# Kernel optimization log

Hardware: AMD Instinct MI355X
Metric: run time of the kernel (lower is better)

Reference implementation:

```python
import jax, jax.numpy as jnp
import numpy as np

COMMITMENT = 0.25
THRESHOLD = 0.6
SNR_DB = 30.0  # eval_snr_db default-ish channel condition (fixed for determinism)
LN_EPS = 1e-5


def _layernorm(x, g, b):
    m = jnp.mean(x, axis=-1, keepdims=True)
    v = jnp.var(x, axis=-1, keepdims=True)
    return (x - m) * jax.lax.rsqrt(v + LN_EPS) * g + b


def _vq(x, codebook):
    # x: [T, D], codebook: [K, D]. Nearest-neighbor quantize + per-token VQ loss + STE.
    d = (x * x).sum(-1, keepdims=True) - 2.0 * (x @ codebook.T) + (codebook * codebook).sum(-1)  # [T, K]
    idx = jnp.argmin(d, axis=-1)
    q = codebook[idx]  # [T, D]
    loss = (COMMITMENT * jnp.mean((x - jax.lax.stop_gradient(q)) ** 2, axis=-1)
            + jnp.mean((jax.lax.stop_gradient(x) - q) ** 2, axis=-1))  # [T]
    q_ste = x + jax.lax.stop_gradient(q - x)
    return q_ste, loss


def setup_inputs() -> dict:
    key = jax.random.key(0)
    ks = jax.random.split(key, 8)
    B, N, De, Dq, Dd = 64, 196, 768, 512, 256
    return {
        'x_tokens': jax.random.normal(ks[0], (B, N, De), jnp.float32),
        'fim_logits': jax.random.normal(ks[1], (B, N, 1), jnp.float32),
        'W_proj': jax.random.normal(ks[2], (De, Dq), jnp.float32) * (1.0 / np.sqrt(De)),
        'b_proj': jnp.zeros((Dq,), jnp.float32),
        'ln_g': jnp.ones((Dq,), jnp.float32),
        'ln_b': jnp.zeros((Dq,), jnp.float32),
        'cb_high': jax.random.normal(ks[3], (4096, Dq), jnp.float32),
        'cb_low': jax.random.normal(ks[4], (256, Dq), jnp.float32),
        'W_dec': jax.random.normal(ks[5], (Dq, Dd), jnp.float32) * (1.0 / np.sqrt(Dq)),
        'b_dec': jnp.zeros((Dd,), jnp.float32),
        'h_ri': jax.random.normal(ks[6], (B, 2), jnp.float32),
        'noise': jax.random.normal(ks[7], (B, N, Dq), jnp.float32),
    }


def reference(x_tokens, fim_logits, W_proj, b_proj, ln_g, ln_b, cb_high, cb_low, W_dec, b_dec, h_ri, noise):
    B, N, _ = x_tokens.shape
    score = jax.nn.sigmoid(fim_logits[..., 0])          # [B, N]
    route_high = score > THRESHOLD                       # [B, N] bool

    x_proj = _layernorm(x_tokens @ W_proj + b_proj, ln_g, ln_b)  # [B, N, Dq]
    D = x_proj.shape[-1]
    xf = x_proj.reshape(-1, D)
    mf = route_high.reshape(-1)
    sf = score.reshape(-1)

    # Compute both experts densely, select with mask (same math as the masked
    # gather/scatter dispatch in the torch code, jit-friendly static shapes).
    q_high, loss_high = _vq(xf, cb_high)
    q_low, loss_low = _vq(xf, cb_low)
    final = jnp.where(mf[:, None], q_high, q_low).reshape(B, N, D)

    n_high = jnp.maximum(mf.sum(), 1)
    n_low = jnp.maximum((~mf).sum(), 1)
    vq_loss = (jnp.sum(jnp.where(mf, loss_high * sf, 0.0)) / n_high
               + jnp.sum(jnp.where(mf, 0.0, loss_low * (1.0 - sf))) / n_low) / 2.0

    # Rayleigh channel: per-sample fading magnitude h = |CN(0,1)|/sqrt(2), AWGN, equalize.
    n_var = 10.0 ** (-SNR_DB / 10.0)
    h = jnp.sqrt((h_ri ** 2).sum(-1)) / jnp.sqrt(2.0)    # [B]
    h = h[:, None, None]
    y = (h * final + jnp.sqrt(n_var) * noise) / h

    x_dec = y @ W_dec + b_dec                            # [B, N, 256]
    return x_dec, vq_loss
```

## Files before the change

### kernel.cpp

```cpp
#include <hip/hip_runtime.h>
#include <math.h>

#define T_TOK 12544
#define DE 768
#define DQ 512
#define DD 256
#define SEQ 196
#define NCH 4096
#define NCL 256
#define SPL_H 16
#define CODES_PER_BLK 256
#define MARGIN 2.0f
#define CAND_CAP 16

typedef __attribute__((ext_vector_type(8))) short s16x8;
typedef __attribute__((ext_vector_type(4))) float f32x4;

__device__ __forceinline__ float wave_reduce_sum(float v) {
    #pragma unroll
    for (int off = 32; off > 0; off >>= 1) v += __shfl_xor(v, off);
    return v;
}

__device__ __forceinline__ unsigned short f2bf(float f) {
    unsigned int u = __float_as_uint(f);
    u = (u + 0x7fffu + ((u >> 16) & 1u)) >> 16;
    return (unsigned short)u;
}
__device__ __forceinline__ float bf2f(unsigned short h) {
    return __uint_as_float(((unsigned int)h) << 16);
}

__device__ __forceinline__ void sumsq_body(const float* __restrict__ cb,
                                           float* __restrict__ cs2,
                                           unsigned short* __restrict__ cbB,
                                           int blk, int NC) {
    int row = blk * 4 + (threadIdx.x >> 6);
    int lane = threadIdx.x & 63;
    if (row >= NC) return;
    const float4* p = (const float4*)(cb + (size_t)row * DQ);
    float4 a = p[lane];
    float4 b = p[lane + 64];
    if (cbB) {
        unsigned short* dst = cbB + (size_t)row * DQ;
        ushort4 ha, hb;
        ha.x = f2bf(a.x); ha.y = f2bf(a.y); ha.z = f2bf(a.z); ha.w = f2bf(a.w);
        hb.x = f2bf(b.x); hb.y = f2bf(b.y); hb.z = f2bf(b.z); hb.w = f2bf(b.w);
        *(ushort4*)(dst + lane * 4) = ha;
        *(ushort4*)(dst + 256 + lane * 4) = hb;
    }
    float s = a.x*a.x + a.y*a.y + a.z*a.z + a.w*a.w
            + b.x*b.x + b.y*b.y + b.z*b.z + b.w*b.w;
    s = wave_reduce_sum(s);
    if (lane == 0) cs2[row] = s;
}

__device__ __forceinline__ void split_body(const float* __restrict__ W, int K, int N,
                                           unsigned short* __restrict__ Thi,
                                           unsigned short* __restrict__ Tlo,
                                           int blk, int nb) {
    int total = K * N;
    for (int idx = blk * 256 + threadIdx.x; idx < total; idx += nb * 256) {
        int n = idx / K, k = idx - n * K;
        float v = W[(size_t)k * N + n];
        unsigned short h = f2bf(v);
        Thi[idx] = h;
        Tlo[idx] = f2bf(v - bf2f(h));
    }
}

__global__ __launch_bounds__(256) void prep_all(const float* __restrict__ cb_h,
                                                float* __restrict__ cs2h,
                                                unsigned short* __restrict__ cbhB,
                                                const float* __restrict__ cb_l,
                                                float* __restrict__ cs2l,
                                                unsigned short* __restrict__ cblB,
                                                const float* __restrict__ Wp,
                                                unsigned short* __restrict__ WThi,
                                                unsigned short* __restrict__ WTlo,
                                                const float* __restrict__ Wd,
                                                unsigned short* __restrict__ WdThi,
                                                unsigned short* __restrict__ WdTlo) {
    int blk = blockIdx.x;
    if (blk < 1024)       sumsq_body(cb_h, cs2h, cbhB, blk, NCH);
    else if (blk < 1088)  sumsq_body(cb_l, cs2l, cblB, blk - 1024, NCL);
    else if (blk < 1600)  split_body(Wp, DE, DQ, WThi, WTlo, blk - 1088, 512);
    else                  split_body(Wd, DQ, DD, WdThi, WdTlo, blk - 1600, 256);
}

template<int NC>
__global__ __launch_bounds__(256) void code_sumsq(const float* __restrict__ cb,
                                                  float* __restrict__ cs2) {
    sumsq_body(cb, cs2, nullptr, blockIdx.x, NC);
}

template<int KDIM, int NSTRIDE, int BN>
__global__ __launch_bounds__(256) void gemm_mfma3(const float* __restrict__ A,
                                                  const unsigned short* __restrict__ BThi,
                                                  const unsigned short* __restrict__ BTlo,
                                                  const float* __restrict__ bias,
                                                  float* __restrict__ out) {
    constexpr int CPW = BN / 64;
    __shared__ __align__(16) unsigned short Ahi[2][64 * 32];
    __shared__ __align__(16) unsigned short Alo[2][64 * 32];
    __shared__ __align__(16) unsigned short Bhi[2][BN * 32];
    __shared__ __align__(16) unsigned short Blo[2][BN * 32];
    const int m0 = blockIdx.x * 64, n0 = blockIdx.y * BN;
    const int tid = threadIdx.x, lane = tid & 63, w = tid >> 6;
    const int stok = tid >> 2, sslot = tid & 3;

    f32x4 acc[4][CPW] = {};
    float4 av0, av1;
    uint4 bh4[CPW], bl4[CPW];

    auto loadStep = [&](int k0) {
        const float* src = A + (size_t)(m0 + stok) * KDIM + k0 + sslot * 8;
        av0 = *(const float4*)src;
        av1 = *(const float4*)(src + 4);
        #pragma unroll
        for (int c = 0; c < CPW; c++) {
            size_t soff = (size_t)(n0 + c * 64 + stok) * KDIM + k0 + sslot * 8;
            bh4[c] = *(const uint4*)(BThi + soff);
            bl4[c] = *(const uint4*)(BTlo + soff);
        }
    };
    auto writeStep = [&](int buf) {
        float xv[8] = {av0.x, av0.y, av0.z, av0.w, av1.x, av1.y, av1.z, av1.w};
        unsigned int hw[4], lw[4];
        #pragma unroll
        for (int j = 0; j < 4; j++) {
            unsigned short h0 = f2bf(xv[2*j]),   h1 = f2bf(xv[2*j+1]);
            unsigned short l0 = f2bf(xv[2*j] - bf2f(h0));
            unsigned short l1 = f2bf(xv[2*j+1] - bf2f(h1));
            hw[j] = (unsigned)h0 | ((unsigned)h1 << 16);
            lw[j] = (unsigned)l0 | ((unsigned)l1 << 16);
        }
        int doffA = stok * 32 + (sslot ^ ((stok >> 1) & 3)) * 8;
        *(uint4*)&Ahi[buf][doffA] = make_uint4(hw[0], hw[1], hw[2], hw[3]);
        *(uint4*)&Alo[buf][doffA] = make_uint4(lw[0], lw[1], lw[2], lw[3]);
        #pragma unroll
        for (int c = 0; c < CPW; c++) {
            int col = c * 64 + stok;
            int doffB = col * 32 + (sslot ^ ((col >> 1) & 3)) * 8;
            *(uint4*)&Bhi[buf][doffB] = bh4[c];
            *(uint4*)&Blo[buf][doffB] = bl4[c];
        }
    };

    loadStep(0); writeStep(0); __syncthreads();
    const int NT = KDIM / 32;
    for (int t = 0; t < NT; t++) {
        const int cur = t & 1;
        if (t + 1 < NT) loadStep((t + 1) * 32);
        const int fr = lane & 15, fs = lane >> 4;
        s16x8 ah[4], al[4];
        #pragma unroll
        for (int tm = 0; tm < 4; tm++) {
            int tok = tm * 16 + fr;
            int off = tok * 32 + (fs ^ ((tok >> 1) & 3)) * 8;
            ah[tm] = *(const s16x8*)&Ahi[cur][off];
            al[tm] = *(const s16x8*)&Alo[cur][off];
        }
        #pragma unroll
        for (int n = 0; n < CPW; n++) {
            int col = w * (16 * CPW) + n * 16 + fr;
            int boff = col * 32 + (fs ^ ((col >> 1) & 3)) * 8;
            s16x8 bh = *(const s16x8*)&Bhi[cur][boff];
            s16x8 bl = *(const s16x8*)&Blo[cur][boff];
            #pragma unroll
            for (int tm = 0; tm < 4; tm++) {
                acc[tm][n] = __builtin_amdgcn_mfma_f32_16x16x32_bf16(ah[tm], bh, acc[tm][n], 0, 0, 0);
                acc[tm][n] = __builtin_amdgcn_mfma_f32_16x16x32_bf16(ah[tm], bl, acc[tm][n], 0, 0, 0);
                acc[tm][n] = __builtin_amdgcn_mfma_f32_16x16x32_bf16(al[tm], bh, acc[tm][n], 0, 0, 0);
            }
        }
        if (t + 1 < NT) writeStep(cur ^ 1);
        __syncthreads();
    }
    const int fr = lane & 15, fg = lane >> 4;
    #pragma unroll
    for (int n = 0; n < CPW; n++) {
        const int col = n0 + w * (16 * CPW) + n * 16 + fr;
        const float bb = bias[col];
        #pragma unroll
        for (int tm = 0; tm < 4; tm++) {
            #pragma unroll
            for (int r = 0; r < 4; r++) {
                int row = m0 + tm * 16 + fg * 4 + r;
                out[(size_t)row * NSTRIDE + col] = acc[tm][n][r] + bb;
            }
        }
    }
}

__global__ __launch_bounds__(256) void proj_gemm(const float* __restrict__ X,
                                                 const float* __restrict__ W,
                                                 const float* __restrict__ bias,
                                                 float* __restrict__ out) {
    __shared__ float As[32][66];
    __shared__ float Bs[32][64];
    const int m0 = blockIdx.x * 64, n0 = blockIdx.y * 64;
    const int tid = threadIdx.x;
    const int tx = tid & 15, ty = tid >> 4;
    float acc[4][4] = {};
    for (int k0 = 0; k0 < DE; k0 += 32) {
        {
            int e = tid;
            int r = e >> 3, c4 = e & 7;
            float4 v = *(const float4*)(X + (size_t)(m0 + r) * DE + k0 + c4 * 4);
            As[c4*4+0][r] = v.x; As[c4*4+1][r] = v.y; As[c4*4+2][r] = v.z; As[c4*4+3][r] = v.w;
            e = tid + 256;
            r = e >> 3; c4 = e & 7;
            v = *(const float4*)(X + (size_t)(m0 + r) * DE + k0 + c4 * 4);
            As[c4*4+0][r] = v.x; As[c4*4+1][r] = v.y; As[c4*4+2][r] = v.z; As[c4*4+3][r] = v.w;
        }
        {
            int e = tid;
            int kk = e >> 4, c4 = e & 15;
            *(float4*)&Bs[kk][c4*4] = *(const float4*)(W + (size_t)(k0 + kk) * DQ + n0 + c4 * 4);
            e = tid + 256;
            kk = e >> 4; c4 = e & 15;
            *(float4*)&Bs[kk][c4*4] = *(const float4*)(W + (size_t)(k0 + kk) * DQ + n0 + c4 * 4);
        }
        __syncthreads();
        #pragma unroll
        for (int k = 0; k < 32; k++) {
            float2 a01 = *(const float2*)&As[k][ty * 4];
            float2 a23 = *(const float2*)&As[k][ty * 4 + 2];
            float4 b = *(const float4*)&Bs[k][tx * 4];
            float av[4] = {a01.x, a01.y, a23.x, a23.y};
            float bv[4] = {b.x, b.y, b.z, b.w};
            #pragma unroll
            for (int i = 0; i < 4; i++)
                #pragma unroll
                for (int j = 0; j < 4; j++)
                    acc[i][j] += av[i] * bv[j];
        }
        __syncthreads();
    }
    float4 bv4 = *(const float4*)(bias + n0 + tx * 4);
    float bb[4] = {bv4.x, bv4.y, bv4.z, bv4.w};
    #pragma unroll
    for (int i = 0; i < 4; i++) {
        int row = m0 + ty * 4 + i;
        float4 o;
        o.x = acc[i][0] + bb[0];
        o.y = acc[i][1] + bb[1];
        o.z = acc[i][2] + bb[2];
        o.w = acc[i][3] + bb[3];
        *(float4*)(out + (size_t)row * DQ + n0 + tx * 4) = o;
    }
}

__global__ __launch_bounds__(256) void ln_route(float* __restrict__ xp,
                                                const float* __restrict__ g,
                                                const float* __restrict__ b,
                                                const float* __restrict__ logits,
                                                float* __restrict__ score,
                                                int* __restrict__ mask,
                                                unsigned short* __restrict__ xpB) {
    int row = blockIdx.x * 4 + (threadIdx.x >> 6);
    int lane = threadIdx.x & 63;
    float* p = xp + (size_t)row * DQ;
    float4 v0 = *(float4*)(p + lane * 4);
    float4 v1 = *(float4*)(p + 256 + lane * 4);
    float s  = v0.x + v0.y + v0.z + v0.w + v1.x + v1.y + v1.z + v1.w;
    float ss = v0.x*v0.x + v0.y*v0.y + v0.z*v0.z + v0.w*v0.w
             + v1.x*v1.x + v1.y*v1.y + v1.z*v1.z + v1.w*v1.w;
    s = wave_reduce_sum(s);
    ss = wave_reduce_sum(ss);
    float m = s * (1.f / DQ);
    float var = ss * (1.f / DQ) - m * m;
    float scale = rsqrtf(var + 1e-5f);
    float4 g0 = *(const float4*)(g + lane * 4);
    float4 g1 = *(const float4*)(g + 256 + lane * 4);
    float4 b0 = *(const float4*)(b + lane * 4);
    float4 b1 = *(const float4*)(b + 256 + lane * 4);
    float4 o0, o1;
    o0.x = (v0.x - m) * scale * g0.x + b0.x;
    o0.y = (v0.y - m) * scale * g0.y + b0.y;
    o0.z = (v0.z - m) * scale * g0.z + b0.z;
    o0.w = (v0.w - m) * scale * g0.w + b0.w;
    o1.x = (v1.x - m) * scale * g1.x + b1.x;
    o1.y = (v1.y - m) * scale * g1.y + b1.y;
    o1.z = (v1.z - m) * scale * g1.z + b1.z;
    o1.w = (v1.w - m) * scale * g1.w + b1.w;
    *(float4*)(p + lane * 4) = o0;
    *(float4*)(p + 256 + lane * 4) = o1;
    if (xpB) {
        unsigned short* dst = xpB + (size_t)row * DQ;
        ushort4 h0, h1;
        h0.x = f2bf(o0.x); h0.y = f2bf(o0.y); h0.z = f2bf(o0.z); h0.w = f2bf(o0.w);
        h1.x = f2bf(o1.x); h1.y = f2bf(o1.y); h1.z = f2bf(o1.z); h1.w = f2bf(o1.w);
        *(ushort4*)(dst + lane * 4) = h0;
        *(ushort4*)(dst + 256 + lane * 4) = h1;
    }
    if (lane == 0) {
        float lg = logits[row];
        float sc = 1.f / (1.f + expf(-lg));
        score[row] = sc;
        mask[row] = sc > 0.6f ? 1 : 0;
    }
}

__global__ __launch_bounds__(1024) void scan_compact(const int* __restrict__ mask,
                                                     int* __restrict__ hlist,
                                                     int* __restrict__ llist,
                                                     int* __restrict__ counts) {
    __shared__ int wsum[16];
    __shared__ int base_h, base_l;
    int tid = threadIdx.x, lane = tid & 63, wid = tid >> 6;
    if (tid == 0) { base_h = 0; base_l = 0; }
    __syncthreads();
    for (int t0 = 0; t0 < T_TOK; t0 += 1024) {
        int t = t0 + tid;
        int valid = t < T_TOK;
        int m = valid ? mask[t] : 0;
        unsigned long long bal = __ballot(m);
        int pre = __popcll(bal & ((1ull << lane) - 1ull));
        if (lane == 0) wsum[wid] = __popcll(bal);
        __syncthreads();
        int woff = 0;
        for (int w = 0; w < wid; w++) woff += wsum[w];
        int btot = 0;
        for (int w = 0; w < 16; w++) btot += wsum[w];
        int vcnt = T_TOK - t0; if (vcnt > 1024) vcnt = 1024;
        int bh = base_h, bl = base_l;
        if (valid) {
            if (m) hlist[bh + woff + pre] = t;
            else   llist[bl + (tid - (woff + pre))] = t;
        }
        __syncthreads();
        if (tid == 0) { base_h = bh + btot; base_l = bl + (vcnt - btot); }
        __syncthreads();
    }
    if (tid == 0) { counts[0] = base_h; counts[1] = base_l; }
}

__global__ __launch_bounds__(256) void vq_mfma_all(const unsigned short* __restrict__ xpB,
                                                   const unsigned short* __restrict__ cbhB,
                                                   const float* __restrict__ cs2h,
                                                   const int* __restrict__ hlist,
                                                   const unsigned short* __restrict__ cblB,
                                                   const float* __restrict__ cs2l,
                                                   const int* __restrict__ llist,
                                                   const int* __restrict__ counts,
                                                   float* __restrict__ smaxH,
                                                   int* __restrict__ scntH,
                                                   uint2* __restrict__ candH,
                                                   float* __restrict__ smaxL,
                                                   int* __restrict__ scntL,
                                                   uint2* __restrict__ candL) {
    const int by = blockIdx.y;
    const unsigned short* cbB; const float* cs2; const int* list;
    float* smax; int* scnt; uint2* cand;
    int count, slice, SPLIT;
    if (by < SPL_H) {
        cbB = cbhB; cs2 = cs2h; list = hlist; count = counts[0];
        slice = by; SPLIT = SPL_H; smax = smaxH; scnt = scntH; cand = candH;
    } else {
        cbB = cblB; cs2 = cs2l; list = llist; count = counts[1];
        slice = 0; SPLIT = 1; smax = smaxL; scnt = scntL; cand = candL;
    }
    const int base = blockIdx.x * 64;
    if (base >= count) return;
    const int cbase = slice * CODES_PER_BLK;

    __shared__ __align__(16) unsigned short Abuf[2][64 * 32];
    __shared__ __align__(16) unsigned short Bbuf[2][256 * 32];
    __shared__ float wmaxs[4][64];
    __shared__ float tokmax[64];
    __shared__ int ccnt[64];
    __shared__ uint2 cland[64][CAND_CAP];
    __shared__ int rows_s[64];

    const int tid = threadIdx.x;
    const int lane = tid & 63;
    const int w = tid >> 6;

    if (tid < 64) {
        int tl = base + tid;
        rows_s[tid] = list[tl < count ? tl : (count - 1)];
        ccnt[tid] = 0;
    }
    __syncthreads();

    f32x4 acc[4][4] = {};

    const int stok = tid >> 2, sslot = tid & 3;
    for (int k0 = 0; k0 < DQ; k0 += 64) {
        if (k0) __syncthreads();
        #pragma unroll
        for (int h = 0; h < 2; h++) {
            uint4 v = *(const uint4*)(xpB + (size_t)rows_s[stok] * DQ + k0 + h * 32 + sslot * 8);
            *(uint4*)&Abuf[h][stok * 32 + (sslot ^ ((stok >> 1) & 3)) * 8] = v;
            #pragma unroll
            for (int cc = 0; cc < 4; cc++) {
                int code = cc * 64 + stok;
                uint4 bv = *(const uint4*)(cbB + (size_t)(cbase + code) * DQ + k0 + h * 32 + sslot * 8);
                *(uint4*)&Bbuf[h][code * 32 + (sslot ^ ((code >> 1) & 3)) * 8] = bv;
            }
        }
        __syncthreads();
        const int fr = lane & 15, fs = lane >> 4;
        #pragma unroll
        for (int h = 0; h < 2; h++) {
            s16x8 af[4], bf[4];
            #pragma unroll
            for (int tm = 0; tm < 4; tm++) {
                int tok = tm * 16 + fr;
                af[tm] = *(const s16x8*)&Abuf[h][tok * 32 + (fs ^ ((tok >> 1) & 3)) * 8];
            }
            #pragma unroll
            for (int tn = 0; tn < 4; tn++) {
                int cl = w * 64 + tn * 16 + fr;
                bf[tn] = *(const s16x8*)&Bbuf[h][cl * 32 + (fs ^ ((cl >> 1) & 3)) * 8];
            }
            #pragma unroll
            for (int tm = 0; tm < 4; tm++)
                #pragma unroll
                for (int tn = 0; tn < 4; tn++)
                    acc[tm][tn] = __builtin_amdgcn_mfma_f32_16x16x32_bf16(af[tm], bf[tn], acc[tm][tn], 0, 0, 0);
        }
    }
    __syncthreads();

    const int fr = lane & 15, fg = lane >> 4;
    float c2[4];
    #pragma unroll
    for (int tn = 0; tn < 4; tn++) c2[tn] = 0.5f * cs2[cbase + w * 64 + tn * 16 + fr];

    #pragma unroll
    for (int tm = 0; tm < 4; tm++) {
        #pragma unroll
        for (int r = 0; r < 4; r++) {
            float m4 = -3.0e38f;
            #pragma unroll
            for (int tn = 0; tn < 4; tn++) {
                float s = acc[tm][tn][r] - c2[tn];
                m4 = fmaxf(m4, s);
            }
            #pragma unroll
            for (int off = 1; off < 16; off <<= 1)
                m4 = fmaxf(m4, __shfl_xor(m4, off));
            if (fr == 0) wmaxs[w][tm * 16 + fg * 4 + r] = m4;
        }
    }
    __syncthreads();
    if (tid < 64)
        tokmax[tid] = fmaxf(fmaxf(wmaxs[0][tid], wmaxs[1][tid]),
                            fmaxf(wmaxs[2][tid], wmaxs[3][tid]));
    __syncthreads();

    #pragma unroll
    for (int tm = 0; tm < 4; tm++) {
        #pragma unroll
        for (int r = 0; r < 4; r++) {
            int token = tm * 16 + fg * 4 + r;
            float thr = tokmax[token] - MARGIN;
            #pragma unroll
            for (int tn = 0; tn < 4; tn++) {
                float s = acc[tm][tn][r] - c2[tn];
                if (s > thr) {
                    int pos = atomicAdd(&ccnt[token], 1);
                    if (pos < CAND_CAP) {
                        uint2 cd;
                        cd.x = __float_as_uint(s);
                        cd.y = (unsigned)(cbase + w * 64 + tn * 16 + fr);
                        cland[token][pos] = cd;
                    }
                }
            }
        }
    }
    __syncthreads();

    if (tid < 64) {
        int tl = base + tid;
        if (tl < count) {
            smax[(size_t)tl * SPLIT + slice] = tokmax[tid];
            scnt[(size_t)tl * SPLIT + slice] = min(ccnt[tid], CAND_CAP);
        }
    }
    for (int i = tid; i < 64 * CAND_CAP; i += 256) {
        int token = i >> 4, j = i & (CAND_CAP - 1);
        int tl = base + token;
        if (tl < count && j < min(ccnt[token], CAND_CAP))
            cand[((size_t)tl * SPLIT + slice) * CAND_CAP + j] = cland[token][j];
    }
}

__global__ __launch_bounds__(256) void vq_rescore_all(float* __restrict__ xp,
                                                      const float* __restrict__ cb_h,
                                                      const float* __restrict__ smaxH,
                                                      const int* __restrict__ scntH,
                                                      const uint2* __restrict__ candH,
                                                      const int* __restrict__ hlist,
                                                      const float* __restrict__ cb_l,
                                                      const float* __restrict__ smaxL,
                                                      const int* __restrict__ scntL,
                                                      const uint2* __restrict__ candL,
                                                      const int* __restrict__ llist,
                                                      const int* __restrict__ counts,
                                                      int* __restrict__ out_idx,
                                                      const float* __restrict__ noise,
                                                      const float* __restrict__ h_ri,
                                                      const float* __restrict__ score,
                                                      float* __restrict__ lh,
                                                      float* __restrict__ ll) {
    const int HB = T_TOK / 4;
    int bx = blockIdx.x;
    const float* cb; const float* smax; const int* scnt; const uint2* cand; const int* list;
    int count, SPLIT, cidx;
    if (bx < HB) {
        cb = cb_h; smax = smaxH; scnt = scntH; cand = candH; list = hlist;
        count = counts[0]; SPLIT = SPL_H; cidx = 0;
    } else {
        bx -= HB;
        cb = cb_l; smax = smaxL; scnt = scntL; cand = candL; list = llist;
        count = counts[1]; SPLIT = 1; cidx = 1;
    }
    const int wid = threadIdx.x >> 6;
    const int lane = threadIdx.x & 63;
    const int tl = bx * 4 + wid;
    if (tl >= count) return;

    float gm = -3.0e38f;
    if (lane < SPLIT) gm = smax[(size_t)tl * SPLIT + lane];
    #pragma unroll
    for (int off = 1; off < 64; off <<= 1)
        gm = fmaxf(gm, __shfl_xor(gm, off));
    const float thr = gm - MARGIN;

    const int t = list[tl];
    float xv[8];
    #pragma unroll
    for (int kk = 0; kk < 8; kk++) xv[kk] = xp[(size_t)t * DQ + lane * 8 + kk];

    double bs = -1.0e300;
    int bi = 0x7fffffff;
    for (int s = 0; s < SPLIT; s++) {
        int cn = scnt[(size_t)tl * SPLIT + s];
        for (int j = 0; j < cn; j++) {
            uint2 cd = cand[((size_t)tl * SPLIT + s) * CAND_CAP + j];
            float av = __uint_as_float(cd.x);
            if (av >= thr) {
                int code = (int)cd.y;
                const float* crow = cb + (size_t)code * DQ;
                double dot = 0.0, nrm = 0.0;
                #pragma unroll
                for (int kk = 0; kk < 8; kk++) {
                    double cv = (double)crow[lane * 8 + kk];
                    dot += (double)xv[kk] * cv;
                    nrm += cv * cv;
                }
                #pragma unroll
                for (int off = 1; off < 64; off <<= 1) {
                    dot += __shfl_xor(dot, off);
                    nrm += __shfl_xor(nrm, off);
                }
                double sc = dot - 0.5 * nrm;
                if (sc > bs || (sc == bs && code < bi)) { bs = sc; bi = code; }
            }
        }
    }
    const float* qrow = cb + (size_t)bi * DQ;
    float4 q0 = *(const float4*)(qrow + lane * 8);
    float4 q1 = *(const float4*)(qrow + lane * 8 + 4);
    const float* nz = noise + (size_t)t * DQ;
    float4 n0 = *(const float4*)(nz + lane * 8);
    float4 n1 = *(const float4*)(nz + lane * 8 + 4);
    float ds = 0.f, dx;
    dx = xv[0] - q0.x; ds += dx * dx;
    dx = xv[1] - q0.y; ds += dx * dx;
    dx = xv[2] - q0.z; ds += dx * dx;
    dx = xv[3] - q0.w; ds += dx * dx;
    dx = xv[4] - q1.x; ds += dx * dx;
    dx = xv[5] - q1.y; ds += dx * dx;
    dx = xv[6] - q1.z; ds += dx * dx;
    dx = xv[7] - q1.w; ds += dx * dx;
    ds = wave_reduce_sum(ds);
    int bbt = t / SEQ;
    float hh0 = h_ri[bbt * 2], hh1 = h_ri[bbt * 2 + 1];
    float hh = sqrtf((hh0 * hh0 + hh1 * hh1) * 0.5f);
    float cc = sqrtf(1e-3f) / hh;
    float4 y0, y1;
    y0.x = q0.x + cc * n0.x; y0.y = q0.y + cc * n0.y;
    y0.z = q0.z + cc * n0.z; y0.w = q0.w + cc * n0.w;
    y1.x = q1.x + cc * n1.x; y1.y = q1.y + cc * n1.y;
    y1.z = q1.z + cc * n1.z; y1.w = q1.w + cc * n1.w;
    *(float4*)(xp + (size_t)t * DQ + lane * 8) = y0;
    *(float4*)(xp + (size_t)t * DQ + lane * 8 + 4) = y1;
    if (lane == 0) {
        out_idx[t] = bi;
        float loss = 1.25f * ds * (1.f / DQ);
        float sc = score[t];
        if (cidx == 0) { lh[t] = loss * sc;  ll[t] = 0.f; }
        else           { lh[t] = 0.f;        ll[t] = loss * (1.f - sc); }
    }
}

template<int NC, int SPLIT>
__global__ __launch_bounds__(256) void vq_partial(const float* __restrict__ xp,
                                                  const float* __restrict__ cb,
                                                  const float* __restrict__ cs2,
                                                  const int* __restrict__ list,
                                                  const int* __restrict__ counts,
                                                  int cidx,
                                                  float* __restrict__ part_s,
                                                  int* __restrict__ part_i) {
    const int count = counts[cidx];
    const int base = blockIdx.x * 64;
    if (base >= count) return;
    const int CODES = NC / SPLIT;
    const int cbase = blockIdx.y * CODES;
    __shared__ float As[32][68];
    __shared__ float Cs[32][68];
    __shared__ int rows_s[64];
    const int tid = threadIdx.x;
    if (tid < 64) {
        int tl = base + tid;
        rows_s[tid] = list[tl < count ? tl : (count - 1)];
    }
    __syncthreads();
    const int tx = tid & 15, ty = tid >> 4;
    float best_s[4];
    int best_i[4];
    #pragma unroll
    for (int i = 0; i < 4; i++) { best_s[i] = -3.0e38f; best_i[i] = 0; }
    for (int c0 = cbase; c0 < cbase + CODES; c0 += 64) {
        float acc[4][4] = {};
        for (int k0 = 0; k0 < DQ; k0 += 32) {
            {
                int e = tid;
                int r = e >> 3, c4 = e & 7;
                float4 v = *(const float4*)(xp + (size_t)rows_s[r] * DQ + k0 + c4 * 4);
                As[c4*4+0][r] = v.x; As[c4*4+1][r] = v.y; As[c4*4+2][r] = v.z; As[c4*4+3][r] = v.w;
                e = tid + 256; r = e >> 3; c4 = e & 7;
                v = *(const float4*)(xp + (size_t)rows_s[r] * DQ + k0 + c4 * 4);
                As[c4*4+0][r] = v.x; As[c4*4+1][r] = v.y; As[c4*4+2][r] = v.z; As[c4*4+3][r] = v.w;
            }
            {
                int e = tid;
                int r = e >> 3, c4 = e & 7;
                float4 v = *(const float4*)(cb + (size_t)(c0 + r) * DQ + k0 + c4 * 4);
                Cs[c4*4+0][r] = v.x; Cs[c4*4+1][r] = v.y; Cs[c4*4+2][r] = v.z; Cs[c4*4+3][r] = v.w;
                e = tid + 256; r = e >> 3; c4 = e & 7;
                v = *(const float4*)(cb + (size_t)(c0 + r) * DQ + k0 + c4 * 4);
                Cs[c4*4+0][r] = v.x; Cs[c4*4+1][r] = v.y; Cs[c4*4+2][r] = v.z; Cs[c4*4+3][r] = v.w;
            }
            __syncthreads();
            #pragma unroll
            for (int k = 0; k < 32; k++) {
                float4 a = *(const float4*)&As[k][ty * 4];
                float4 b = *(const float4*)&Cs[k][tx * 4];
                float av[4] = {a.x, a.y, a.z, a.w};
                float bv[4] = {b.x, b.y, b.z, b.w};
                #pragma unroll
                for (int i = 0; i < 4; i++)
                    #pragma unroll
                    for (int j = 0; j < 4; j++)
                        acc[i][j] += av[i] * bv[j];
            }
            __syncthreads();
        }
        float4 c2v = *(const float4*)(cs2 + c0 + tx * 4);
        float c2[4] = {c2v.x, c2v.y, c2v.z, c2v.w};
        #pragma unroll
        for (int i = 0; i < 4; i++) {
            float s = acc[i][0] - 0.5f * c2[0];
            int bi = c0 + tx * 4;
            #pragma unroll
            for (int j = 1; j < 4; j++) {
                float sj = acc[i][j] - 0.5f * c2[j];
                if (sj > s) { s = sj; bi = c0 + tx * 4 + j; }
            }
            #pragma unroll
            for (int off = 1; off < 16; off <<= 1) {
                float os = __shfl_xor(s, off);
                int oi = __shfl_xor(bi, off);
                if (os > s || (os == s && oi < bi)) { s = os; bi = oi; }
            }
            if (s > best_s[i] || (s == best_s[i] && bi < best_i[i])) {
                best_s[i] = s; best_i[i] = bi;
            }
        }
    }
    if (tx == 0) {
        #pragma unroll
        for (int i = 0; i < 4; i++) {
            int tl = base + ty * 4 + i;
            if (tl < count) {
                part_s[(size_t)tl * SPLIT + blockIdx.y] = best_s[i];
                part_i[(size_t)tl * SPLIT + blockIdx.y] = best_i[i];
            }
        }
    }
}

template<int SPLIT>
__global__ __launch_bounds__(256) void vq_reduce(const float* __restrict__ part_s,
                                                 const int* __restrict__ part_i,
                                                 const int* __restrict__ list,
                                                 const int* __restrict__ counts,
                                                 int cidx,
                                                 int* __restrict__ out_idx) {
    int tl = blockIdx.x * 256 + threadIdx.x;
    if (tl >= counts[cidx]) return;
    float bs = part_s[(size_t)tl * SPLIT];
    int bi = part_i[(size_t)tl * SPLIT];
    #pragma unroll
    for (int s = 1; s < SPLIT; s++) {
        float v = part_s[(size_t)tl * SPLIT + s];
        int vi = part_i[(size_t)tl * SPLIT + s];
        if (v > bs || (v == bs && vi < bi)) { bs = v; bi = vi; }
    }
    out_idx[list[tl]] = bi;
}

__global__ __launch_bounds__(256) void gather_loss_y(float* __restrict__ xp,
                                                     const float* __restrict__ cb_h,
                                                     const float* __restrict__ cb_l,
                                                     const int* __restrict__ idx,
                                                     const float* __restrict__ score,
                                                     const int* __restrict__ mask,
                                                     const float* __restrict__ noise,
                                                     const float* __restrict__ h_ri,
                                                     float* __restrict__ lh,
                                                     float* __restrict__ ll) {
    int t = blockIdx.x * 4 + (threadIdx.x >> 6);
    int lane = threadIdx.x & 63;
    int m = mask[t];
    float sc = score[t];
    const float* q = (m ? cb_h : cb_l) + (size_t)idx[t] * DQ;
    float* x = xp + (size_t)t * DQ;
    const float* nz = noise + (size_t)t * DQ;
    int bb = t / SEQ;
    float h0 = h_ri[bb * 2], h1 = h_ri[bb * 2 + 1];
    float h = sqrtf((h0 * h0 + h1 * h1) * 0.5f);
    float c = sqrtf(1e-3f) / h;
    float4 xv0 = *(float4*)(x + lane * 4);
    float4 xv1 = *(float4*)(x + 256 + lane * 4);
    float4 qv0 = *(const float4*)(q + lane * 4);
    float4 qv1 = *(const float4*)(q + 256 + lane * 4);
    float4 nv0 = *(const float4*)(nz + lane * 4);
    float4 nv1 = *(const float4*)(nz + 256 + lane * 4);
    float dx, ds = 0.f;
    dx = xv0.x - qv0.x; ds += dx * dx;
    dx = xv0.y - qv0.y; ds += dx * dx;
    dx = xv0.z - qv0.z; ds += dx * dx;
    dx = xv0.w - qv0.w; ds += dx * dx;
    dx = xv1.x - qv1.x; ds += dx * dx;
    dx = xv1.y - qv1.y; ds += dx * dx;
    dx = xv1.z - qv1.z; ds += dx * dx;
    dx = xv1.w - qv1.w; ds += dx * dx;
    ds = wave_reduce_sum(ds);
    float4 y0, y1;
    y0.x = qv0.x + c * nv0.x; y0.y = qv0.y + c * nv0.y;
    y0.z = qv0.z + c * nv0.z; y0.w = qv0.w + c * nv0.w;
    y1.x = qv1.x + c * nv1.x; y1.y = qv1.y + c * nv1.y;
    y1.z = qv1.z + c * nv1.z; y1.w = qv1.w + c * nv1.w;
    *(float4*)(x + lane * 4) = y0;
    *(float4*)(x + 256 + lane * 4) = y1;
    if (lane == 0) {
        float loss = 1.25f * ds * (1.f / DQ);
        lh[t] = m ? loss * sc : 0.f;
        ll[t] = m ? 0.f : loss * (1.f - sc);
    }
}

__global__ __launch_bounds__(256) void loss_reduce(const float* __restrict__ lh,
                                                   const float* __restrict__ ll,
                                                   const int* __restrict__ counts,
                                                   float* __restrict__ out) {
    __shared__ float sh[256], sl[256];
    int tid = threadIdx.x;
    float ah = 0.f, al = 0.f;
    for (int t = tid; t < T_TOK; t += 256) { ah += lh[t]; al += ll[t]; }
    sh[tid] = ah; sl[tid] = al;
    __syncthreads();
    for (int o = 128; o > 0; o >>= 1) {
        if (tid < o) { sh[tid] += sh[tid + o]; sl[tid] += sl[tid + o]; }
        __syncthreads();
    }
    if (tid == 0) {
        int nh = counts[0];
        int nl = T_TOK - nh;
        nh = nh > 1 ? nh : 1;
        nl = nl > 1 ? nl : 1;
        out[(size_t)T_TOK * DD] = 0.5f * (sh[0] / (float)nh + sl[0] / (float)nl);
    }
}

__global__ __launch_bounds__(256) void dec_gemm(const float* __restrict__ Y,
                                                const float* __restrict__ W,
                                                const float* __restrict__ bias,
                                                float* __restrict__ out) {
    __shared__ float As[32][66];
    __shared__ float Bs[32][64];
    const int m0 = blockIdx.x * 64, n0 = blockIdx.y * 64;
    const int tid = threadIdx.x;
    const int tx = tid & 15, ty = tid >> 4;
    float acc[4][4] = {};
    for (int k0 = 0; k0 < DQ; k0 += 32) {
        {
            int e = tid;
            int r = e >> 3, c4 = e & 7;
            float4 v = *(const float4*)(Y + (size_t)(m0 + r) * DQ + k0 + c4 * 4);
            As[c4*4+0][r] = v.x; As[c4*4+1][r] = v.y; As[c4*4+2][r] = v.z; As[c4*4+3][r] = v.w;
            e = tid + 256; r = e >> 3; c4 = e & 7;
            v = *(const float4*)(Y + (size_t)(m0 + r) * DQ + k0 + c4 * 4);
            As[c4*4+0][r] = v.x; As[c4*4+1][r] = v.y; As[c4*4+2][r] = v.z; As[c4*4+3][r] = v.w;
        }
        {
            int e = tid;
            int kk = e >> 4, c4 = e & 15;
            *(float4*)&Bs[kk][c4*4] = *(const float4*)(W + (size_t)(k0 + kk) * DD + n0 + c4 * 4);
            e = tid + 256; kk = e >> 4; c4 = e & 15;
            *(float4*)&Bs[kk][c4*4] = *(const float4*)(W + (size_t)(k0 + kk) * DD + n0 + c4 * 4);
        }
        __syncthreads();
        #pragma unroll
        for (int k = 0; k < 32; k++) {
            float2 a01 = *(const float2*)&As[k][ty * 4];
            float2 a23 = *(const float2*)&As[k][ty * 4 + 2];
            float4 b = *(const float4*)&Bs[k][tx * 4];
            float av[4] = {a01.x, a01.y, a23.x, a23.y};
            float bv[4] = {b.x, b.y, b.z, b.w};
            #pragma unroll
            for (int i = 0; i < 4; i++)
                #pragma unroll
                for (int j = 0; j < 4; j++)
                    acc[i][j] += av[i] * bv[j];
        }
        __syncthreads();
    }
    float4 bv4 = *(const float4*)(bias + n0 + tx * 4);
    float bbv[4] = {bv4.x, bv4.y, bv4.z, bv4.w};
    #pragma unroll
    for (int i = 0; i < 4; i++) {
        int row = m0 + ty * 4 + i;
        float4 o;
        o.x = acc[i][0] + bbv[0];
        o.y = acc[i][1] + bbv[1];
        o.z = acc[i][2] + bbv[2];
        o.w = acc[i][3] + bbv[3];
        *(float4*)(out + (size_t)row * DD + n0 + tx * 4) = o;
    }
}

extern "C" void kernel_launch(void* const* d_in, const int* in_sizes, int n_in,
                              void* d_out, int out_size, void* d_ws, size_t ws_size,
                              hipStream_t stream) {
    const float* x_tokens = (const float*)d_in[0];
    const float* fim      = (const float*)d_in[1];
    const float* W_proj   = (const float*)d_in[2];
    const float* b_proj   = (const float*)d_in[3];
    const float* ln_g     = (const float*)d_in[4];
    const float* ln_b     = (const float*)d_in[5];
    const float* cb_high  = (const float*)d_in[6];
    const float* cb_low   = (const float*)d_in[7];
    const float* W_dec    = (const float*)d_in[8];
    const float* b_dec    = (const float*)d_in[9];
    const float* h_ri     = (const float*)d_in[10];
    const float* noise    = (const float*)d_in[11];
    float* out = (float*)d_out;

    char* ws = (char*)d_ws;
    size_t off = 0;
    float* xp = (float*)(ws + off);     off += (size_t)T_TOK * DQ * 4;
    int*   idxb = (int*)(ws + off);     off += (size_t)T_TOK * 4;
    float* score = (float*)(ws + off);  off += (size_t)T_TOK * 4;
    int*   mask = (int*)(ws + off);     off += (size_t)T_TOK * 4;
    float* lh = (float*)(ws + off);     off += (size_t)T_TOK * 4;
    float* ll = (float*)(ws + off);     off += (size_t)T_TOK * 4;
    int*   hlist = (int*)(ws + off);    off += (size_t)T_TOK * 4;
    int*   llist = (int*)(ws + off);    off += (size_t)T_TOK * 4;
    int*   counts = (int*)(ws + off);   off += 64;
    float* cs2h = (float*)(ws + off);   off += (size_t)NCH * 4;
    float* cs2l = (float*)(ws + off);   off += (size_t)NCL * 4;
    size_t off_common = off;

    unsigned short* xpB  = (unsigned short*)(ws + off); off += (size_t)T_TOK * DQ * 2;
    unsigned short* cbhB = (unsigned short*)(ws + off); off += (size_t)NCH * DQ * 2;
    unsigned short* cblB = (unsigned short*)(ws + off); off += (size_t)NCL * DQ * 2;
    float* smaxH = (float*)(ws + off);  off += (size_t)T_TOK * SPL_H * 4;
    int*   scntH = (int*)(ws + off);    off += (size_t)T_TOK * SPL_H * 4;
    uint2* candH = (uint2*)(ws + off);  off += (size_t)T_TOK * SPL_H * CAND_CAP * 8;
    float* smaxL = (float*)(ws + off);  off += (size_t)T_TOK * 4;
    int*   scntL = (int*)(ws + off);    off += (size_t)T_TOK * 4;
    uint2* candL = (uint2*)(ws + off);  off += (size_t)T_TOK * CAND_CAP * 8;
    unsigned short* WThi  = (unsigned short*)(ws + off); off += (size_t)DQ * DE * 2;
    unsigned short* WTlo  = (unsigned short*)(ws + off); off += (size_t)DQ * DE * 2;
    unsigned short* WdThi = (unsigned short*)(ws + off); off += (size_t)DD * DQ * 2;
    unsigned short* WdTlo = (unsigned short*)(ws + off); off += (size_t)DD * DQ * 2;
    size_t need_new = off;
    const bool use_mfma = ws_size >= need_new;

    if (use_mfma) {
        prep_all<<<1856, 256, 0, stream>>>(cb_high, cs2h, cbhB, cb_low, cs2l, cblB,
                                           W_proj, WThi, WTlo, W_dec, WdThi, WdTlo);
        gemm_mfma3<DE, DQ, 64><<<dim3(T_TOK / 64, DQ / 64), 256, 0, stream>>>(
            x_tokens, WThi, WTlo, b_proj, xp);
        ln_route<<<T_TOK / 4, 256, 0, stream>>>(xp, ln_g, ln_b, fim, score, mask, xpB);
        scan_compact<<<1, 1024, 0, stream>>>(mask, hlist, llist, counts);
        vq_mfma_all<<<dim3(T_TOK / 64, SPL_H + 1), 256, 0, stream>>>(
            xpB, cbhB, cs2h, hlist, cblB, cs2l, llist, counts,
            smaxH, scntH, candH, smaxL, scntL, candL);
        vq_rescore_all<<<2 * (T_TOK / 4), 256, 0, stream>>>(
            xp, cb_high, smaxH, scntH, candH, hlist,
            cb_low, smaxL, scntL, candL, llist,
            counts, idxb, noise, h_ri, score, lh, ll);
        loss_reduce<<<1, 256, 0, stream>>>(lh, ll, counts, out);
        gemm_mfma3<DQ, DD, 64><<<dim3(T_TOK / 64, DD / 64), 256, 0, stream>>>(
            xp, WdThi, WdTlo, b_dec, out);
    } else {
        code_sumsq<NCH><<<NCH / 4, 256, 0, stream>>>(cb_high, cs2h);
        code_sumsq<NCL><<<NCL / 4, 256, 0, stream>>>(cb_low, cs2l);
        proj_gemm<<<dim3(T_TOK / 64, DQ / 64), 256, 0, stream>>>(x_tokens, W_proj, b_proj, xp);
        ln_route<<<T_TOK / 4, 256, 0, stream>>>(xp, ln_g, ln_b, fim, score, mask, nullptr);
        scan_compact<<<1, 1024, 0, stream>>>(mask, hlist, llist, counts);
        float* part_s = (float*)(ws + off_common);
        int*   part_i = (int*)(ws + off_common + (size_t)T_TOK * 16 * 4);
        vq_partial<NCH, 16><<<dim3(T_TOK / 64, 16), 256, 0, stream>>>(
            xp, cb_high, cs2h, hlist, counts, 0, part_s, part_i);
        vq_reduce<16><<<(T_TOK + 255) / 256, 256, 0, stream>>>(part_s, part_i, hlist, counts, 0, idxb);
        vq_partial<NCL, 4><<<dim3(T_TOK / 64, 4), 256, 0, stream>>>(
            xp, cb_low, cs2l, llist, counts, 1, part_s, part_i);
        vq_reduce<4><<<(T_TOK + 255) / 256, 256, 0, stream>>>(part_s, part_i, llist, counts, 1, idxb);
        gather_loss_y<<<T_TOK / 4, 256, 0, stream>>>(xp, cb_high, cb_low, idxb, score, mask,
                                                     noise, h_ri, lh, ll);
        loss_reduce<<<1, 256, 0, stream>>>(lh, ll, counts, out);
        dec_gemm<<<dim3(T_TOK / 64, DD / 64), 256, 0, stream>>>(xp, W_dec, b_dec, out);
    }
}
```

Before: 215.7 us.

## Stage VQ GEMM tiles with direct global-to-LDS loads and double buffering

Result: no change. 217.5 us (+0.8%).

```diff
diff --git a/kernel.cpp b/kernel.cpp
--- a/kernel.cpp
+++ b/kernel.cpp
@@ -29,6 +29,13 @@
 }
 __device__ __forceinline__ float bf2f(unsigned short h) {
     return __uint_as_float(((unsigned int)h) << 16);
+}
+
+__device__ __forceinline__ void gload_lds16(const unsigned short* g, unsigned short* l) {
+    __builtin_amdgcn_global_load_lds(
+        (const __attribute__((address_space(1))) void*)g,
+        (__attribute__((address_space(3))) void*)l,
+        16, 0, 0);
 }
 
 __device__ __forceinline__ void sumsq_body(const float* __restrict__ cb,
@@ -366,8 +373,8 @@
     if (base >= count) return;
     const int cbase = slice * CODES_PER_BLK;
 
-    __shared__ __align__(16) unsigned short Abuf[2][64 * 32];
-    __shared__ __align__(16) unsigned short Bbuf[2][256 * 32];
+    __shared__ __align__(16) unsigned short Abuf[2 * 64 * 32];
+    __shared__ __align__(16) unsigned short Bbuf[2 * 256 * 32];
     __shared__ float wmaxs[4][64];
     __shared__ float tokmax[64];
     __shared__ int ccnt[64];
@@ -377,6 +384,7 @@
     const int tid = threadIdx.x;
     const int lane = tid & 63;
     const int w = tid >> 6;
+    const int stok = tid >> 2, sslot = tid & 3;
 
     if (tid < 64) {
         int tl = base + tid;
@@ -385,45 +393,50 @@
     }
     __syncthreads();
 
+    const int swz = sslot ^ ((stok >> 1) & 3);
+    const unsigned short* gA  = xpB + (size_t)rows_s[stok] * DQ + swz * 8;
+    const unsigned short* gB0 = cbB + (size_t)(cbase + 0 * 64 + stok) * DQ + swz * 8;
+    const unsigned short* gB1 = cbB + (size_t)(cbase + 1 * 64 + stok) * DQ + swz * 8;
+    const unsigned short* gB2 = cbB + (size_t)(cbase + 2 * 64 + stok) * DQ + swz * 8;
+    const unsigned short* gB3 = cbB + (size_t)(cbase + 3 * 64 + stok) * DQ + swz * 8;
+    unsigned short* dA = Abuf + w * 512;
+    unsigned short* dB = Bbuf + w * 512;
+
+    auto stage = [&](int buf, int k0) {
+        gload_lds16(gA  + k0, dA + buf * (64 * 32));
+        gload_lds16(gB0 + k0, dB + buf * (256 * 32) + 0 * 2048);
+        gload_lds16(gB1 + k0, dB + buf * (256 * 32) + 1 * 2048);
+        gload_lds16(gB2 + k0, dB + buf * (256 * 32) + 2 * 2048);
+        gload_lds16(gB3 + k0, dB + buf * (256 * 32) + 3 * 2048);
+    };
+
     f32x4 acc[4][4] = {};
 
-    const int stok = tid >> 2, sslot = tid & 3;
-    for (int k0 = 0; k0 < DQ; k0 += 64) {
-        if (k0) __syncthreads();
-        #pragma unroll
-        for (int h = 0; h < 2; h++) {
-            uint4 v = *(const uint4*)(xpB + (size_t)rows_s[stok] * DQ + k0 + h * 32 + sslot * 8);
-            *(uint4*)&Abuf[h][stok * 32 + (sslot ^ ((stok >> 1) & 3)) * 8] = v;
-            #pragma unroll
-            for (int cc = 0; cc < 4; cc++) {
-                int code = cc * 64 + stok;
-                uint4 bv = *(const uint4*)(cbB + (size_t)(cbase + code) * DQ + k0 + h * 32 + sslot * 8);
-                *(uint4*)&Bbuf[h][code * 32 + (sslot ^ ((code >> 1) & 3)) * 8] = bv;
-            }
-        }
+    stage(0, 0);
+    __syncthreads();
+    const int NT = DQ / 32;
+    for (int t = 0; t < NT; t++) {
+        const int cur = t & 1;
+        if (t + 1 < NT) stage(cur ^ 1, (t + 1) * 32);
+        const int fr = lane & 15, fs = lane >> 4;
+        s16x8 af[4], bf[4];
+        #pragma unroll
+        for (int tm = 0; tm < 4; tm++) {
+            int tok = tm * 16 + fr;
+            af[tm] = *(const s16x8*)&Abuf[cur * (64 * 32) + tok * 32 + (fs ^ ((tok >> 1) & 3)) * 8];
+        }
+        #pragma unroll
+        for (int tn = 0; tn < 4; tn++) {
+            int cl = w * 64 + tn * 16 + fr;
+            bf[tn] = *(const s16x8*)&Bbuf[cur * (256 * 32) + cl * 32 + (fs ^ ((cl >> 1) & 3)) * 8];
+        }
+        #pragma unroll
+        for (int tm = 0; tm < 4; tm++)
+            #pragma unroll
+            for (int tn = 0; tn < 4; tn++)
+                acc[tm][tn] = __builtin_amdgcn_mfma_f32_16x16x32_bf16(af[tm], bf[tn], acc[tm][tn], 0, 0, 0);
         __syncthreads();
-        const int fr = lane & 15, fs = lane >> 4;
-        #pragma unroll
-        for (int h = 0; h < 2; h++) {
-            s16x8 af[4], bf[4];
-            #pragma unroll
-            for (int tm = 0; tm < 4; tm++) {
-                int tok = tm * 16 + fr;
-                af[tm] = *(const s16x8*)&Abuf[h][tok * 32 + (fs ^ ((tok >> 1) & 3)) * 8];
-            }
-            #pragma unroll
-            for (int tn = 0; tn < 4; tn++) {
-                int cl = w * 64 + tn * 16 + fr;
-                bf[tn] = *(const s16x8*)&Bbuf[h][cl * 32 + (fs ^ ((cl >> 1) & 3)) * 8];
-            }
-            #pragma unroll
-            for (int tm = 0; tm < 4; tm++)
-                #pragma unroll
-                for (int tn = 0; tn < 4; tn++)
-                    acc[tm][tn] = __builtin_amdgcn_mfma_f32_16x16x32_bf16(af[tm], bf[tn], acc[tm][tn], 0, 0, 0);
-        }
-    }
-    __syncthreads();
+    }
 
     const int fr = lane & 15, fg = lane >> 4;
     float c2[4];
```
